# Kernel tuning notes

Measured on AMD Instinct MI355X. Metric: run time of the kernel, lower is better.

The kernel has to match this reference:

```python
import jax, jax.numpy as jnp
import numpy as np

B, T, D = 2, 2048, 2048
H, DK = 16, 96
DV = 192                 # head_v_dim = head_dim * expand_v (expand_v=2)
KEY_DIM = H * DK         # 1536 = 0.75*D
VAL_DIM = H * DV         # 3072 = 1.5*D
KS = 4                   # short-conv kernel size
EPS = 1e-6


def setup_inputs() -> dict:
    key = jax.random.key(0)
    ks = jax.random.split(key, 16)
    nrm = lambda k, shape, s: jax.random.normal(k, shape, jnp.float32) * s
    # dt_bias init as in the torch module
    dt_min, dt_max = 1e-3, 1e-1
    dt = jnp.exp(jax.random.uniform(ks[12], (H,), jnp.float32)
                 * (np.log(dt_max) - np.log(dt_min)) + np.log(dt_min))
    dt_bias = dt + jnp.log(-jnp.expm1(-dt))
    return {
        'x': nrm(ks[0], (B, T, D), 1.0),
        'Wq': nrm(ks[1], (D, KEY_DIM), D ** -0.5),
        'Wk': nrm(ks[2], (D, KEY_DIM), D ** -0.5),
        'Wv': nrm(ks[3], (D, VAL_DIM), D ** -0.5),
        'Wb': nrm(ks[4], (D, H), D ** -0.5),
        'Wa': nrm(ks[5], (D, H), D ** -0.5),
        'Wg': nrm(ks[6], (D, VAL_DIM), D ** -0.5),
        'Wo': nrm(ks[7], (VAL_DIM, D), VAL_DIM ** -0.5),
        'conv_q_w': nrm(ks[8], (KEY_DIM, KS), KS ** -0.5),
        'conv_k_w': nrm(ks[9], (KEY_DIM, KS), KS ** -0.5),
        'conv_v_w': nrm(ks[10], (VAL_DIM, KS), KS ** -0.5),
        'A_log': jnp.log(jax.random.uniform(ks[11], (H,), jnp.float32, 1e-4, 16.0)),
        'dt_bias': dt_bias,
        'o_norm_weight': jnp.ones((DV,), jnp.float32),
    }


def _causal_depthwise_conv(x, w):
    # x: (B, T, C), w: (C, KS). Depthwise causal conv + SiLU.
    xp = jnp.pad(x, ((0, 0), (KS - 1, 0), (0, 0)))
    y = sum(xp[:, j:j + T, :] * w[:, j] for j in range(KS))
    return jax.nn.silu(y)


def _gated_delta_scan(q, k, v, g, beta):
    # q,k: (B,T,H,DK)  v: (B,T,H,DV)  g,beta: (B,T,H)
    def step(S, inp):
        q_t, k_t, v_t, g_t, b_t = inp          # (B,H,DK),(B,H,DK),(B,H,DV),(B,H),(B,H)
        alpha = jnp.exp(g_t)                   # (B,H)
        retrieved = jnp.einsum('bhk,bhkv->bhv', k_t, S)
        error = v_t - retrieved                # (B,H,DV)
        S = alpha[:, :, None, None] * S + b_t[:, :, None, None] * (
            k_t[:, :, :, None] * error[:, :, None, :])
        o_t = jnp.einsum('bhk,bhkv->bhv', q_t, S)
        return S, o_t

    tm = lambda a: jnp.swapaxes(a, 0, 1)       # time-major
    S0 = jnp.zeros((B, H, DK, DV), jnp.float32)
    _, o = jax.lax.scan(step, S0, (tm(q), tm(k), tm(v), tm(g), tm(beta)))
    return jnp.swapaxes(o, 0, 1)               # (B,T,H,DV)


def reference(x, Wq, Wk, Wv, Wb, Wa, Wg, Wo,
              conv_q_w, conv_k_w, conv_v_w, A_log, dt_bias, o_norm_weight):
    # projections + causal depthwise short conv + SiLU
    q = _causal_depthwise_conv(x @ Wq, conv_q_w).reshape(B, T, H, DK)
    k = _causal_depthwise_conv(x @ Wk, conv_k_w).reshape(B, T, H, DK)
    v = _causal_depthwise_conv(x @ Wv, conv_v_w).reshape(B, T, H, DV)

    beta = jax.nn.sigmoid(x @ Wb)                                   # (B,T,H)
    g = -jnp.exp(A_log) * jax.nn.softplus(x @ Wa + dt_bias)         # (B,T,H)

    # qk L2 normalization (use_qk_l2norm_in_kernel=True path)
    q = q * jax.lax.rsqrt(jnp.sum(q * q, -1, keepdims=True) + 1e-12)
    k = k * jax.lax.rsqrt(jnp.sum(k * k, -1, keepdims=True) + 1e-12)

    o = _gated_delta_scan(q, k, v, g, beta)                         # (B,T,H,DV)

    # gated RMSNorm over head_v_dim
    g_out = (x @ Wg).reshape(B, T, H, DV)
    rms = jax.lax.rsqrt(jnp.mean(o * o, -1, keepdims=True) + EPS)
    o = (o * rms) * o_norm_weight * jax.nn.sigmoid(g_out)

    return o.reshape(B, T, VAL_DIM) @ Wo                            # (B,T,D)
```

## Files before the change

kernel.cpp:

```cpp
#include <hip/hip_runtime.h>

#define B_ 2
#define T_ 2048
#define D_ 2048
#define H_ 16
#define DK_ 96
#define DV_ 192
#define KEYD 1536
#define VALD 3072
#define NPROJ 9216
#define PQK 6144
#define KS_ 4
#define C_ 64
#define NC_ 32

typedef unsigned short u16;
typedef unsigned int u32;
typedef __bf16 bf16x8 __attribute__((ext_vector_type(8)));
typedef float f32x4 __attribute__((ext_vector_type(4)));

__device__ __forceinline__ u16 f2bf(float f) {
  unsigned u = __float_as_uint(f);
  u += 0x7FFF + ((u >> 16) & 1);
  return (u16)(u >> 16);
}
__device__ __forceinline__ float bf2f(u16 v) { return __uint_as_float((unsigned)v << 16); }
__device__ __forceinline__ float bflo(u32 w) { return __uint_as_float(w << 16); }
__device__ __forceinline__ float bfhi(u32 w) { return __uint_as_float(w & 0xFFFF0000u); }

__device__ __forceinline__ void gll16(const void* g, void* lds) {
  __builtin_amdgcn_global_load_lds(
      (const __attribute__((address_space(1))) void*)g,
      (__attribute__((address_space(3))) void*)lds, 16, 0, 0);
}

__global__ __launch_bounds__(256) void cast_x(const float* __restrict__ in,
                                              u16* __restrict__ out, int n4) {
  int i = blockIdx.x * 256 + threadIdx.x;
  if (i < n4) {
    float4 v = reinterpret_cast<const float4*>(in)[i];
    ushort4 o;
    o.x = f2bf(v.x); o.y = f2bf(v.y); o.z = f2bf(v.z); o.w = f2bf(v.w);
    reinterpret_cast<ushort4*>(out)[i] = o;
  }
}

__device__ __forceinline__ void tc_body(const float* __restrict__ src,
                                        u16* __restrict__ dst, int R, int C,
                                        int bx, int by, int tid) {
  __shared__ float tile[32][33];
  int tx = tid & 31, ty = tid >> 5;
  int c0 = bx * 32, r0 = by * 32;
#pragma unroll
  for (int j = 0; j < 4; ++j)
    tile[ty + j * 8][tx] = src[(size_t)(r0 + ty + j * 8) * C + c0 + tx];
  __syncthreads();
#pragma unroll
  for (int j = 0; j < 4; ++j)
    dst[(size_t)(c0 + ty + j * 8) * R + r0 + tx] = f2bf(tile[tx][ty + j * 8]);
}

__global__ __launch_bounds__(256) void transpose_cast(const float* __restrict__ src,
                                                      u16* __restrict__ dst, int R, int C) {
  tc_body(src, dst, R, C, blockIdx.x, blockIdx.y, threadIdx.x);
}

__global__ __launch_bounds__(256) void transpose_cast4(const float* __restrict__ Wq,
    const float* __restrict__ Wk, const float* __restrict__ Wv,
    const float* __restrict__ Wg, u16* __restrict__ WT) {
  int id = blockIdx.x;
  if (id < 3072) {
    tc_body(Wq, WT, 2048, 1536, id % 48, id / 48, threadIdx.x);
  } else if (id < 6144) {
    id -= 3072;
    tc_body(Wk, WT + (size_t)1536 * 2048, 2048, 1536, id % 48, id / 48, threadIdx.x);
  } else if (id < 12288) {
    id -= 6144;
    tc_body(Wv, WT + (size_t)3072 * 2048, 2048, 3072, id % 96, id / 96, threadIdx.x);
  } else {
    id -= 12288;
    tc_body(Wg, WT + (size_t)6144 * 2048, 2048, 3072, id % 96, id / 96, threadIdx.x);
  }
}

template <int OUT16>
__global__ __launch_bounds__(512, 2) void gemm256(const u16* __restrict__ A,
    const u16* __restrict__ BT, u16* __restrict__ C0, u16* __restrict__ C1,
    float* __restrict__ Cf, int M, int N, int K, int nsplit, int s0, int s1) {
  __shared__ u16 LA[2][256 * 64];
  __shared__ u16 LB[2][256 * 64];
  const int tid = threadIdx.x, wave = tid >> 6, lane = tid & 63;
  const int l15 = lane & 15, l16 = lane >> 4, x7 = l15 & 7;
  const int wr = wave >> 2, wc = wave & 3;
  const int m0 = blockIdx.y * 256, n0 = blockIdx.x * 256;
  const int r8 = lane >> 3;
  const int csrc = ((lane & 7) ^ r8) << 3;
  const int NKT = K >> 6;
  f32x4 acc[8][4] = {};

#define STG_A(p, kt, half) { \
    const u16* As_ = A + (size_t)m0 * K + (size_t)(kt) * 64; \
    _Pragma("unroll") \
    for (int g = 0; g < 2; ++g) { \
      int rowb = g * 128 + (half) * 64 + wave * 8; \
      gll16(As_ + (size_t)(rowb + r8) * K + csrc, (char*)&LA[p][0] + rowb * 128); \
    } \
  }
#define STG_B(p, kt) { \
    const u16* Bs_ = BT + (size_t)n0 * K + (size_t)(kt) * 64; \
    _Pragma("unroll") \
    for (int j = 0; j < 4; ++j) { \
      int rowb = j * 64 + wave * 8; \
      gll16(Bs_ + (size_t)(rowb + r8) * K + csrc, (char*)&LB[p][0] + rowb * 128); \
    } \
  }

#define LDA8(p, mh, dst) { \
    _Pragma("unroll") \
    for (int mi = 0; mi < 4; ++mi) \
      _Pragma("unroll") \
      for (int kk = 0; kk < 2; ++kk) { \
        int row = wr * 128 + (mh) * 64 + mi * 16 + l15; \
        dst[mi * 2 + kk] = *(const bf16x8*)((const char*)&LA[p][0] + row * 128 + (((kk * 4 + l16) ^ x7) << 4)); \
      } \
  }
#define LDB4(p, nh, dst) { \
    _Pragma("unroll") \
    for (int ni = 0; ni < 2; ++ni) \
      _Pragma("unroll") \
      for (int kk = 0; kk < 2; ++kk) { \
        int row = wc * 64 + (nh) * 32 + ni * 16 + l15; \
        dst[ni * 2 + kk] = *(const bf16x8*)((const char*)&LB[p][0] + row * 128 + (((kk * 4 + l16) ^ x7) << 4)); \
      } \
  }

#define MMQ(AF, BF, mbase, nbase) { \
    __builtin_amdgcn_s_setprio(1); \
    _Pragma("unroll") \
    for (int mi = 0; mi < 4; ++mi) \
      _Pragma("unroll") \
      for (int ni = 0; ni < 2; ++ni) \
        _Pragma("unroll") \
        for (int kk = 0; kk < 2; ++kk) \
          acc[(mbase) + mi][(nbase) + ni] = __builtin_amdgcn_mfma_f32_16x16x32_bf16( \
              AF[mi * 2 + kk], BF[ni * 2 + kk], acc[(mbase) + mi][(nbase) + ni], 0, 0, 0); \
    __builtin_amdgcn_s_setprio(0); \
  }

#define BARR() __builtin_amdgcn_s_barrier()

  STG_A(0, 0, 0); STG_A(0, 0, 1); STG_B(0, 0);
  if (NKT > 1) {
    STG_A(1, 1, 0); STG_A(1, 1, 1); STG_B(1, 1);
    asm volatile("s_waitcnt vmcnt(8)" ::: "memory");
  } else {
    asm volatile("s_waitcnt vmcnt(0)" ::: "memory");
  }
  BARR();

  bf16x8 afA[8], afB[8], bf0[4], bf1[4];
  for (int c = 0; c < NKT; ++c) {
    const int p = c & 1;
    const bool stg = (c + 2 < NKT);
    LDA8(p, 0, afA); LDB4(p, 0, bf0);
    BARR();
    MMQ(afA, bf0, 0, 0);
    BARR();
    LDB4(p, 1, bf1);
    if (stg) STG_A(p, c + 2, 0);
    BARR();
    MMQ(afA, bf1, 0, 2);
    BARR();
    LDA8(p, 1, afB);
    if (stg) STG_B(p, c + 2);
    BARR();
    MMQ(afB, bf1, 4, 2);
    BARR();
    if (stg) {
      STG_A(p, c + 2, 1);
      asm volatile("s_waitcnt vmcnt(8)" ::: "memory");
    } else if (c + 1 < NKT) {
      asm volatile("s_waitcnt vmcnt(0)" ::: "memory");
    }
    BARR();
    MMQ(afB, bf0, 4, 0);
    BARR();
  }

#pragma unroll
  for (int mi = 0; mi < 8; ++mi)
#pragma unroll
    for (int ni = 0; ni < 4; ++ni)
#pragma unroll
      for (int j = 0; j < 4; ++j) {
        int row = m0 + wr * 128 + mi * 16 + l16 * 4 + j;
        int col = n0 + wc * 64 + ni * 16 + l15;
        float v = acc[mi][ni][j];
        if (OUT16) {
          if (col < nsplit) C0[(size_t)row * s0 + col] = f2bf(v);
          else              C1[(size_t)row * s1 + col - nsplit] = f2bf(v);
        } else {
          Cf[(size_t)row * N + col] = v;
        }
      }
#undef STG_A
#undef STG_B
#undef LDA8
#undef LDB4
#undef MMQ
#undef BARR
}

template <int OUT16>
__global__ __launch_bounds__(256) void gemm_bt(const u16* __restrict__ A,
                                               const u16* __restrict__ BT,
                                               u16* __restrict__ C0, u16* __restrict__ C1,
                                               float* __restrict__ Cf,
                                               int M, int N, int K, int nsplit, int s0, int s1) {
  __shared__ u16 As[128 * 32];
  __shared__ u16 Bs[128 * 32];
  int tid = threadIdx.x;
  int wave = tid >> 6, lane = tid & 63;
  int l15 = lane & 15, l16 = lane >> 4;
  int m0 = blockIdx.y * 128, n0 = blockIdx.x * 128;
  int wm = (wave >> 1) * 64, wn = (wave & 1) * 64;
  f32x4 acc[4][4] = {};
  int nkt = K >> 5;
  for (int kt = 0; kt < nkt; ++kt) {
    int k0 = kt << 5;
    __syncthreads();
#pragma unroll
    for (int rr = 0; rr < 2; ++rr) {
      int idx = tid + rr * 256;
      int row = idx >> 2, kc8 = (idx & 3) * 8;
      unsigned loff = (unsigned)(rr * 256 + wave * 64) * 16;
      gll16(A + (size_t)(m0 + row) * K + k0 + kc8, (char*)As + loff);
      gll16(BT + (size_t)(n0 + row) * K + k0 + kc8, (char*)Bs + loff);
    }
    __syncthreads();
    bf16x8 af[4], bfr[4];
#pragma unroll
    for (int i = 0; i < 4; ++i)
      af[i] = *reinterpret_cast<const bf16x8*>(&As[(wm + i * 16 + l15) * 32 + l16 * 8]);
#pragma unroll
    for (int i = 0; i < 4; ++i)
      bfr[i] = *reinterpret_cast<const bf16x8*>(&Bs[(wn + i * 16 + l15) * 32 + l16 * 8]);
#pragma unroll
    for (int mi = 0; mi < 4; ++mi)
#pragma unroll
      for (int ni = 0; ni < 4; ++ni)
        acc[mi][ni] = __builtin_amdgcn_mfma_f32_16x16x32_bf16(af[mi], bfr[ni], acc[mi][ni], 0, 0, 0);
  }
#pragma unroll
  for (int mi = 0; mi < 4; ++mi)
#pragma unroll
    for (int ni = 0; ni < 4; ++ni)
#pragma unroll
      for (int j = 0; j < 4; ++j) {
        int row = m0 + wm + mi * 16 + l16 * 4 + j;
        int col = n0 + wn + ni * 16 + l15;
        if (OUT16) {
          if (col < nsplit) C0[(size_t)row * s0 + col] = f2bf(acc[mi][ni][j]);
          else              C1[(size_t)row * s1 + col - nsplit] = f2bf(acc[mi][ni][j]);
        } else {
          Cf[(size_t)row * N + col] = acc[mi][ni][j];
        }
      }
}

__global__ __launch_bounds__(256) void proj_bg(const float* __restrict__ x,
    const float* __restrict__ Wb, const float* __restrict__ Wa,
    const float* __restrict__ A_log, const float* __restrict__ dt_bias,
    float* __restrict__ beta, float* __restrict__ gg) {
  __shared__ float xs[4 * 2048];
  __shared__ float red[4][32][8];
  int tid = threadIdx.x;
  int r0 = blockIdx.x * 4;
  for (int i = tid; i < 4 * 2048; i += 256)
    xs[i] = x[(size_t)r0 * D_ + i];
  __syncthreads();
  int colg = tid & 31, ks = tid >> 5;
  const float* W = (colg < 16) ? Wb : Wa;
  int wc = colg & 15;
  float p0 = 0, p1 = 0, p2 = 0, p3 = 0;
  int kbeg = ks * 256;
  for (int k = kbeg; k < kbeg + 256; ++k) {
    float wv = W[k * H_ + wc];
    p0 += xs[k] * wv;
    p1 += xs[2048 + k] * wv;
    p2 += xs[4096 + k] * wv;
    p3 += xs[6144 + k] * wv;
  }
  red[0][colg][ks] = p0; red[1][colg][ks] = p1;
  red[2][colg][ks] = p2; red[3][colg][ks] = p3;
  __syncthreads();
  if (tid < 128) {
    int row = tid >> 5, col = tid & 31;
    float d = 0;
#pragma unroll
    for (int i = 0; i < 8; ++i) d += red[row][col][i];
    int r = r0 + row;
    if (col < 16) {
      beta[(size_t)r * H_ + col] = 1.f / (1.f + __expf(-d));
    } else {
      int hh = col - 16;
      float z = d + dt_bias[hh];
      float sp = (z > 20.f) ? z : log1pf(__expf(z));
      gg[(size_t)r * H_ + hh] = -__expf(A_log[hh]) * sp;
    }
  }
}

__global__ __launch_bounds__(256) void conv_qkv(const u16* __restrict__ Pqkv,
    const float* __restrict__ wq, const float* __restrict__ wk, const float* __restrict__ wv,
    u16* __restrict__ qc, u16* __restrict__ kc, u16* __restrict__ vc) {
  __shared__ __align__(16) u16 rows[4][PQK];
  int bt = blockIdx.x;
  int t = bt & (T_ - 1);
  int tid = threadIdx.x, h = tid >> 4, li = tid & 15;
#pragma unroll
  for (int r = 0; r < 4; ++r) {
    bool valid = (t + r - 3) >= 0;
    const uint4* src = (const uint4*)(Pqkv + (ptrdiff_t)(bt + r - 3) * PQK);
    uint4* dst = (uint4*)rows[r];
#pragma unroll
    for (int i = 0; i < 3; ++i) {
      int off = tid + i * 256;
      uint4 v;
      if (valid) v = src[off];
      else { v.x = 0; v.y = 0; v.z = 0; v.w = 0; }
      dst[off] = v;
    }
  }
  __syncthreads();

#pragma unroll
  for (int part = 0; part < 2; ++part) {
    const float* w = part ? wk : wq;
    float y[6]; float ss = 0.f;
#pragma unroll
    for (int jj = 0; jj < 6; ++jj) {
      int c = li + jj * 16;
      int ch = h * DK_ + c;
      float a = 0.f;
#pragma unroll
      for (int j = 0; j < KS_; ++j)
        a += bf2f(rows[j][part * KEYD + ch]) * w[ch * KS_ + j];
      float yv = a / (1.f + __expf(-a));
      y[jj] = yv; ss += yv * yv;
    }
    ss += __shfl_xor(ss, 1); ss += __shfl_xor(ss, 2);
    ss += __shfl_xor(ss, 4); ss += __shfl_xor(ss, 8);
    float rn = rsqrtf(ss + 1e-12f);
    u16* out = (part ? kc : qc) + (size_t)bt * KEYD + h * DK_;
#pragma unroll
    for (int jj = 0; jj < 6; ++jj) out[li + jj * 16] = f2bf(y[jj] * rn);
  }
  u16* vout = vc + (size_t)bt * VALD;
#pragma unroll
  for (int jj = 0; jj < 12; ++jj) {
    int c = tid + jj * 256;
    float a = 0.f;
#pragma unroll
    for (int j = 0; j < KS_; ++j)
      a += bf2f(rows[j][2 * KEYD + c]) * wv[c * KS_ + j];
    vout[c] = f2bf(a / (1.f + __expf(-a)));
  }
}

__global__ __launch_bounds__(320) void chunk_prep(
    const u16* __restrict__ kc, u16* __restrict__ Uv ,
    const float* __restrict__ gg, const float* __restrict__ beta,
    u16* __restrict__ Wg, float* __restrict__ Gcum,
    float* __restrict__ cdArr, float* __restrict__ lamArr) {
  __shared__ __align__(16) u16 ktL[64 * 104];
  __shared__ float AmL[64 * 68];
  __shared__ float glL[64], GclL[64], blL[64], DplL[64];
  int tid = threadIdx.x;
  int flat = blockIdx.x;
  int c = flat & 31, bh = flat >> 5, h = bh & 15, b = bh >> 4;
  int bT0 = b * T_ + c * 64;

  {
    const u32* kg = (const u32*)(kc + (size_t)bT0 * KEYD + h * DK_);
    for (int i = tid; i < 3072; i += 320) {
      int t = i / 48, dd = i - t * 48;
      ((u32*)ktL)[t * 52 + dd] = kg[(size_t)t * (KEYD / 2) + dd];
    }
  }
  if (tid < 64) {
    float g = gg[(size_t)(bT0 + tid) * H_ + h];
    float bv = beta[(size_t)(bT0 + tid) * H_ + h];
    float v = g;
#pragma unroll
    for (int off = 1; off < 64; off <<= 1) {
      float u = __shfl_up(v, off);
      if (tid >= off) v += u;
    }
    float g63 = __shfl(v, 63);
    glL[tid] = g; GclL[tid] = v; blL[tid] = bv; DplL[tid] = __expf(v - g);
    Gcum[(size_t)flat * 64 + tid] = v;
    cdArr[(size_t)flat * 64 + tid] = bv * __expf(g63 - v);
    if (tid == 63) lamArr[flat] = __expf(v);
  }
  __syncthreads();

  {
    int wave = tid >> 6, lane = tid & 63, l15 = lane & 15, l16 = lane >> 4;
    if (wave < 4) {
      f32x4 ac[4] = {};
#pragma unroll
      for (int ks = 0; ks < 3; ++ks) {
        bf16x8 a = *(const bf16x8*)&ktL[(wave * 16 + l15) * 104 + ks * 32 + l16 * 8];
#pragma unroll
        for (int n = 0; n < 4; ++n) {
          bf16x8 bb = *(const bf16x8*)&ktL[(n * 16 + l15) * 104 + ks * 32 + l16 * 8];
          ac[n] = __builtin_amdgcn_mfma_f32_16x16x32_bf16(a, bb, ac[n], 0, 0, 0);
        }
      }
#pragma unroll
      for (int n = 0; n < 4; ++n)
#pragma unroll
        for (int j = 0; j < 4; ++j) {
          int t = wave * 16 + l16 * 4 + j;
          int jj = n * 16 + l15;
          float val = 0.f;
          if (jj < t) val = __expf((GclL[t] - glL[t]) - GclL[jj]) * blL[jj] * ac[n][j];
          AmL[t * 68 + jj] = val;
        }
    }
  }
  __syncthreads();

  if (tid < 288) {
    int j = tid;
    float m[64];
    if (j < 192) {
      const u16* up = Uv + (size_t)bT0 * VALD + h * DV_ + j;
#pragma unroll
      for (int t = 0; t < 64; ++t) m[t] = bf2f(up[(size_t)t * VALD]);
    } else {
      int d = j - 192;
#pragma unroll
      for (int t = 0; t < 64; ++t) m[t] = DplL[t] * bf2f(ktL[t * 104 + d]);
    }
#pragma unroll
    for (int t0 = 0; t0 < 64; t0 += 4) {
      {
        f32x4 a1 = *(const f32x4*)&AmL[(t0 + 1) * 68 + t0];
        m[t0 + 1] -= a1[0] * m[t0];
        f32x4 a2 = *(const f32x4*)&AmL[(t0 + 2) * 68 + t0];
        m[t0 + 2] -= a2[0] * m[t0] + a2[1] * m[t0 + 1];
        f32x4 a3 = *(const f32x4*)&AmL[(t0 + 3) * 68 + t0];
        m[t0 + 3] -= a3[0] * m[t0] + a3[1] * m[t0 + 1] + a3[2] * m[t0 + 2];
      }
#pragma unroll
      for (int tp = t0 + 4; tp < 64; ++tp) {
        f32x4 a = *(const f32x4*)&AmL[tp * 68 + t0];
        m[tp] -= a[0] * m[t0] + a[1] * m[t0 + 1] + a[2] * m[t0 + 2] + a[3] * m[t0 + 3];
      }
    }
    if (j < 192) {
      u16* up = Uv + (size_t)bT0 * VALD + h * DV_ + j;
#pragma unroll
      for (int t = 0; t < 64; ++t) up[(size_t)t * VALD] = f2bf(m[t]);
    } else {
      int d = j - 192;
      u16* wp = Wg + (size_t)bT0 * KEYD + h * DK_ + d;
#pragma unroll
      for (int t = 0; t < 64; ++t) wp[(size_t)t * KEYD] = f2bf(m[t]);
    }
  }
}

__global__ __launch_bounds__(256) void serial_state(
    const u16* __restrict__ kc, const u16* __restrict__ Wg, u16* __restrict__ Ue,
    const float* __restrict__ cdArr, const float* __restrict__ lamArr,
    u16* __restrict__ Schk) {
  __shared__ __align__(16) u16 WtL[2][64 * 104];
  __shared__ __align__(16) u16 ktT[2][96 * 72];
  __shared__ __align__(16) u16 StH[32 * 104];
  __shared__ __align__(16) u16 StLo[32 * 104];
  __shared__ __align__(16) u16 EtH[32 * 72];
  __shared__ __align__(16) u16 EtLo[32 * 72];
  __shared__ float lamS[2];

  int tid = threadIdx.x, wave = tid >> 6, lane = tid & 63;
  int l15 = lane & 15, l16 = lane >> 4;
  int jq = blockIdx.x % 6, bh = blockIdx.x / 6, h = bh & 15, b = bh >> 4;
  int col0 = jq * 32;
  int ntS = wave & 1, m3 = 3 * (wave >> 1);
  int st_t = tid >> 2, st_dd = (tid & 3) * 12;

  f32x4 Sf[3] = {};
  uint4 wreg[3], kreg[3];
  u16 ureg[2][4];
  float cdv[4];
  float lamReg;

#define PREFETCH(bT0p, flatp) { \
    const u32* wgp = (const u32*)(Wg + (size_t)((bT0p) + st_t) * KEYD + h * DK_) + st_dd; \
    const u32* kgp = (const u32*)(kc + (size_t)((bT0p) + st_t) * KEYD + h * DK_) + st_dd; \
    wreg[0] = ((const uint4*)wgp)[0]; wreg[1] = ((const uint4*)wgp)[1]; wreg[2] = ((const uint4*)wgp)[2]; \
    kreg[0] = ((const uint4*)kgp)[0]; kreg[1] = ((const uint4*)kgp)[1]; kreg[2] = ((const uint4*)kgp)[2]; \
    _Pragma("unroll") \
    for (int ni = 0; ni < 2; ++ni) \
      _Pragma("unroll") \
      for (int j = 0; j < 4; ++j) \
        ureg[ni][j] = Ue[(size_t)((bT0p) + wave * 16 + l16 * 4 + j) * VALD + h * DV_ + col0 + ni * 16 + l15]; \
    _Pragma("unroll") \
    for (int j = 0; j < 4; ++j) cdv[j] = cdArr[(size_t)(flatp) * 64 + wave * 16 + l16 * 4 + j]; \
    if (tid == 0) lamReg = lamArr[flatp]; \
  }

  PREFETCH(b * T_, bh * NC_);

  for (int c = 0; c < NC_; ++c) {
    int buf = c & 1;
    int flat = bh * NC_ + c;
    int bT0 = b * T_ + (c << 6);
    {
      u32* wl = (u32*)&WtL[buf][0] + st_t * 52 + st_dd;
      ((uint4*)wl)[0] = wreg[0];
      *(uint4*)(wl + 4) = wreg[1];
      *(uint4*)(wl + 8) = wreg[2];
#pragma unroll
      for (int r = 0; r < 3; ++r) {
        u32 vals[4] = {kreg[r].x, kreg[r].y, kreg[r].z, kreg[r].w};
#pragma unroll
        for (int e = 0; e < 4; ++e) {
          int d = 2 * (st_dd + r * 4 + e);
          ktT[buf][d * 72 + st_t] = (u16)(vals[e] & 0xFFFFu);
          ktT[buf][(d + 1) * 72 + st_t] = (u16)(vals[e] >> 16);
        }
      }
      int cl = ntS * 16 + l15;
      u16* schkRow = Schk + (size_t)flat * (DK_ * DV_) + (size_t)(col0 + cl) * DK_;
#pragma unroll
      for (int i = 0; i < 3; ++i) {
        u16 hi0 = f2bf(Sf[i][0]), hi1 = f2bf(Sf[i][1]);
        u16 hi2 = f2bf(Sf[i][2]), hi3 = f2bf(Sf[i][3]);
        int dbase = (m3 + i) * 16 + l16 * 4;
        StH[cl * 104 + dbase + 0] = hi0; StLo[cl * 104 + dbase + 0] = f2bf(Sf[i][0] - bf2f(hi0));
        StH[cl * 104 + dbase + 1] = hi1; StLo[cl * 104 + dbase + 1] = f2bf(Sf[i][1] - bf2f(hi1));
        StH[cl * 104 + dbase + 2] = hi2; StLo[cl * 104 + dbase + 2] = f2bf(Sf[i][2] - bf2f(hi2));
        StH[cl * 104 + dbase + 3] = hi3; StLo[cl * 104 + dbase + 3] = f2bf(Sf[i][3] - bf2f(hi3));
        u32* ow = (u32*)(schkRow + dbase);
        ow[0] = ((u32)hi1 << 16) | hi0;
        ow[1] = ((u32)hi3 << 16) | hi2;
      }
      if (tid == 0) lamS[buf] = lamReg;
    }
    __syncthreads();
    {
      f32x4 Ea[2] = {};
#pragma unroll
      for (int ks = 0; ks < 3; ++ks) {
        bf16x8 a = *(const bf16x8*)&WtL[buf][(wave * 16 + l15) * 104 + ks * 32 + l16 * 8];
#pragma unroll
        for (int ni = 0; ni < 2; ++ni) {
          bf16x8 bhv = *(const bf16x8*)&StH[(ni * 16 + l15) * 104 + ks * 32 + l16 * 8];
          bf16x8 blv = *(const bf16x8*)&StLo[(ni * 16 + l15) * 104 + ks * 32 + l16 * 8];
          Ea[ni] = __builtin_amdgcn_mfma_f32_16x16x32_bf16(a, bhv, Ea[ni], 0, 0, 0);
          Ea[ni] = __builtin_amdgcn_mfma_f32_16x16x32_bf16(a, blv, Ea[ni], 0, 0, 0);
        }
      }
#pragma unroll
      for (int ni = 0; ni < 2; ++ni)
#pragma unroll
        for (int j = 0; j < 4; ++j) {
          int t = wave * 16 + l16 * 4 + j;
          float ev = bf2f(ureg[ni][j]) - Ea[ni][j];
          Ue[(size_t)(bT0 + t) * VALD + h * DV_ + col0 + ni * 16 + l15] = f2bf(ev);
          float ep = cdv[j] * ev;
          u16 ehi = f2bf(ep);
          int cl = ni * 16 + l15;
          EtH[cl * 72 + t] = ehi;
          EtLo[cl * 72 + t] = f2bf(ep - bf2f(ehi));
        }
      if (c + 1 < NC_) PREFETCH(bT0 + 64, flat + 1);
    }
    __syncthreads();
    {
      float lam = lamS[buf];
#pragma unroll
      for (int i = 0; i < 3; ++i)
#pragma unroll
        for (int j = 0; j < 4; ++j) Sf[i][j] *= lam;
#pragma unroll
      for (int ks = 0; ks < 2; ++ks) {
        bf16x8 bhv = *(const bf16x8*)&EtH[(ntS * 16 + l15) * 72 + ks * 32 + l16 * 8];
        bf16x8 blv = *(const bf16x8*)&EtLo[(ntS * 16 + l15) * 72 + ks * 32 + l16 * 8];
#pragma unroll
        for (int i = 0; i < 3; ++i) {
          bf16x8 a = *(const bf16x8*)&ktT[buf][((m3 + i) * 16 + l15) * 72 + ks * 32 + l16 * 8];
          Sf[i] = __builtin_amdgcn_mfma_f32_16x16x32_bf16(a, bhv, Sf[i], 0, 0, 0);
          Sf[i] = __builtin_amdgcn_mfma_f32_16x16x32_bf16(a, blv, Sf[i], 0, 0, 0);
        }
      }
    }
  }
#undef PREFETCH
}

__global__ __launch_bounds__(256) void chunk_out(
    const u16* __restrict__ qc, const u16* __restrict__ kc, const u16* __restrict__ Ee,
    const u16* __restrict__ Schk, const float* __restrict__ Gcum,
    const float* __restrict__ beta, const u16* __restrict__ Pg,
    const float* __restrict__ onw, u16* __restrict__ onb) {
  __shared__ __align__(16) char pool[65280];
  u16* qL   = (u16*)pool;
  u16* BmL  = (u16*)(pool + 12288);
  u16* BmLo = (u16*)(pool + 21504);
  u16* kL   = (u16*)(pool + 30720);
  u16* StL  = (u16*)(pool + 30720);
  u16* EtL  = (u16*)(pool + 50688);
  float* GclL = (float*)(pool + 64512);
  float* blL  = (float*)(pool + 64768);
  float* DlL  = (float*)(pool + 65024);
  u16* PgL  = (u16*)pool;
  float* wL = (float*)(pool + 24576);

  int tid = threadIdx.x, wave = tid >> 6, lane = tid & 63;
  int l15 = lane & 15, l16 = lane >> 4;
  int flat = blockIdx.x;
  int c = flat & 31, bh = flat >> 5, h = bh & 15, b = bh >> 4;
  int bT0 = b * T_ + c * 64;

  {
    const u32* qg = (const u32*)(qc + (size_t)bT0 * KEYD + h * DK_);
    const u32* kg = (const u32*)(kc + (size_t)bT0 * KEYD + h * DK_);
    for (int i = tid; i < 3072; i += 256) {
      int t = i / 48, dd = i - t * 48;
      ((u32*)qL)[t * 48 + dd] = qg[(size_t)t * (KEYD / 2) + dd];
      ((u32*)kL)[t * 48 + dd] = kg[(size_t)t * (KEYD / 2) + dd];
    }
    if (tid < 64) {
      float gv = Gcum[(size_t)flat * 64 + tid];
      GclL[tid] = gv;
      DlL[tid] = __expf(gv);
      blL[tid] = beta[(size_t)(bT0 + tid) * H_ + h];
    }
  }
  __syncthreads();

  {
    f32x4 bacc[4] = {};
#pragma unroll
    for (int kk = 0; kk < 3; ++kk) {
      bf16x8 aq = *(const bf16x8*)&qL[(wave * 16 + l15) * 96 + kk * 32 + l16 * 8];
#pragma unroll
      for (int n = 0; n < 4; ++n) {
        bf16x8 bk = *(const bf16x8*)&kL[(n * 16 + l15) * 96 + kk * 32 + l16 * 8];
        bacc[n] = __builtin_amdgcn_mfma_f32_16x16x32_bf16(aq, bk, bacc[n], 0, 0, 0);
      }
    }
#pragma unroll
    for (int n = 0; n < 4; ++n)
#pragma unroll
      for (int j = 0; j < 4; ++j) {
        int t = wave * 16 + l16 * 4 + j;
        int jj = n * 16 + l15;
        float val = 0.f;
        if (jj <= t) val = __expf(GclL[t] - GclL[jj]) * blL[jj] * bacc[n][j];
        u16 hi = f2bf(val);
        BmL[t * 72 + jj] = hi;
        BmLo[t * 72 + jj] = f2bf(val - bf2f(hi));
      }
  }
  __syncthreads();

  f32x4 oacc0[6] = {};
  f32x4 oacc1[6] = {};

#define HALFC(half, OACC) { \
    { \
      const u32* sg = (const u32*)(Schk + (size_t)flat * (DK_ * DV_) + (size_t)((half) * 96) * DK_); \
      for (int i = tid; i < 4608; i += 256) { \
        int cL = i / 48, dd = i - cL * 48; \
        ((u32*)&StL[cL * 104])[dd] = sg[cL * 48 + dd]; \
      } \
      const u32* eg = (const u32*)(Ee + (size_t)bT0 * VALD + h * DV_ + (half) * 96); \
      for (int i = tid; i < 3072; i += 256) { \
        int t = i / 48, dd = i - t * 48; \
        u32 w2 = eg[(size_t)t * (VALD / 2) + dd]; \
        EtL[(2 * dd) * 72 + t]     = (u16)(w2 & 0xFFFF); \
        EtL[(2 * dd + 1) * 72 + t] = (u16)(w2 >> 16); \
      } \
    } \
    __syncthreads(); \
    _Pragma("unroll") \
    for (int kk = 0; kk < 3; ++kk) { \
      bf16x8 aq = *(const bf16x8*)&qL[(wave * 16 + l15) * 96 + kk * 32 + l16 * 8]; \
      _Pragma("unroll") \
      for (int n = 0; n < 6; ++n) { \
        bf16x8 bs = *(const bf16x8*)&StL[(n * 16 + l15) * 104 + kk * 32 + l16 * 8]; \
        OACC[n] = __builtin_amdgcn_mfma_f32_16x16x32_bf16(aq, bs, OACC[n], 0, 0, 0); \
      } \
    } \
    _Pragma("unroll") \
    for (int n = 0; n < 6; ++n) \
      _Pragma("unroll") \
      for (int j = 0; j < 4; ++j) \
        OACC[n][j] *= DlL[wave * 16 + l16 * 4 + j]; \
    _Pragma("unroll") \
    for (int kk = 0; kk < 2; ++kk) { \
      bf16x8 ah = *(const bf16x8*)&BmL[(wave * 16 + l15) * 72 + kk * 32 + l16 * 8]; \
      bf16x8 al = *(const bf16x8*)&BmLo[(wave * 16 + l15) * 72 + kk * 32 + l16 * 8]; \
      _Pragma("unroll") \
      for (int n = 0; n < 6; ++n) { \
        bf16x8 be = *(const bf16x8*)&EtL[(n * 16 + l15) * 72 + kk * 32 + l16 * 8]; \
        OACC[n] = __builtin_amdgcn_mfma_f32_16x16x32_bf16(ah, be, OACC[n], 0, 0, 0); \
        OACC[n] = __builtin_amdgcn_mfma_f32_16x16x32_bf16(al, be, OACC[n], 0, 0, 0); \
      } \
    } \
    __syncthreads(); \
  }

  HALFC(0, oacc0);
  HALFC(1, oacc1);
#undef HALFC

  {
    const uint4* pgg = (const uint4*)(Pg + (size_t)bT0 * VALD + h * DV_);
    int tr = tid >> 2, q = tid & 3;
    uint4* dstRow = (uint4*)&PgL[tr * 192];
    const uint4* srcRow = (const uint4*)((const u16*)pgg + (size_t)tr * VALD);
#pragma unroll
    for (int ii = 0; ii < 6; ++ii)
      dstRow[q * 6 + ii] = srcRow[q * 6 + ii];
    if (tid < 192) wL[tid] = onw[tid];
  }
  __syncthreads();

  float ssv[4] = {0.f, 0.f, 0.f, 0.f};
#pragma unroll
  for (int n = 0; n < 6; ++n)
#pragma unroll
    for (int j = 0; j < 4; ++j) {
      float y0 = bf2f(f2bf(oacc0[n][j]));
      float y1 = bf2f(f2bf(oacc1[n][j]));
      ssv[j] += y0 * y0 + y1 * y1;
    }
#pragma unroll
  for (int j = 0; j < 4; ++j) {
    ssv[j] += __shfl_xor(ssv[j], 1); ssv[j] += __shfl_xor(ssv[j], 2);
    ssv[j] += __shfl_xor(ssv[j], 4); ssv[j] += __shfl_xor(ssv[j], 8);
  }
  float rmsv[4];
#pragma unroll
  for (int j = 0; j < 4; ++j) rmsv[j] = rsqrtf(ssv[j] * (1.f / DV_) + 1e-6f);

#define EPIL(OACC, half) { \
    _Pragma("unroll") \
    for (int n = 0; n < 6; ++n) \
      _Pragma("unroll") \
      for (int j = 0; j < 4; ++j) { \
        int t = wave * 16 + l16 * 4 + j; \
        int cc = (half) * 96 + n * 16 + l15; \
        float yv = bf2f(f2bf(OACC[n][j])); \
        float gv = bf2f(PgL[t * 192 + cc]); \
        float sig = 1.f / (1.f + __expf(-gv)); \
        onb[(size_t)(bT0 + t) * VALD + h * DV_ + cc] = f2bf(yv * rmsv[j] * wL[cc] * sig); \
      } \
  }
  EPIL(oacc0, 0);
  EPIL(oacc1, 1);
#undef EPIL
}

extern "C" void kernel_launch(void* const* d_in, const int* in_sizes, int n_in,
                              void* d_out, int out_size, void* d_ws, size_t ws_size,
                              hipStream_t stream) {
  (void)in_sizes; (void)n_in; (void)out_size; (void)ws_size;
  const float* x      = (const float*)d_in[0];
  const float* Wq     = (const float*)d_in[1];
  const float* Wk     = (const float*)d_in[2];
  const float* Wv     = (const float*)d_in[3];
  const float* Wb     = (const float*)d_in[4];
  const float* Wa     = (const float*)d_in[5];
  const float* Wg     = (const float*)d_in[6];
  const float* Wo     = (const float*)d_in[7];
  const float* cqw    = (const float*)d_in[8];
  const float* ckw    = (const float*)d_in[9];
  const float* cvw    = (const float*)d_in[10];
  const float* A_log  = (const float*)d_in[11];
  const float* dt_bias= (const float*)d_in[12];
  const float* onw    = (const float*)d_in[13];
  float* out = (float*)d_out;

  char* ws = (char*)d_ws;
  u16*   xb    = (u16*)  (ws + 0);
  u16*   WT    = (u16*)  (ws + 16777216);
  u16*   qc    = (u16*)  (ws + 0);
  u16*   kc    = (u16*)  (ws + 12582912);
  u16*   vc    = (u16*)  (ws + 25165824);
  u16*   Pqkv  = (u16*)  (ws + 54525952);
  u16*   Wbuf  = (u16*)  (ws + 54525952);
  u16*   Schk  = (u16*)  (ws + 67108864);
  u16*   Pg    = (u16*)  (ws + 104857600);
  float* beta  = (float*)(ws + 155189248);
  float* gg    = (float*)(ws + 155451392);
  float* Gcum  = (float*)(ws + 155713536);
  float* cdArr = (float*)(ws + 155975680);
  float* lamArr= (float*)(ws + 156237824);
  u16*   onb   = (u16*)  (ws + 54525952);
  u16*   WoT   = (u16*)  (ws + 79691776);

  int n4 = B_ * T_ * D_ / 4;
  cast_x<<<(n4 + 255) / 256, 256, 0, stream>>>(x, xb, n4);
  transpose_cast4<<<18432, 256, 0, stream>>>(Wq, Wk, Wv, Wg, WT);

  gemm256<1><<<dim3(NPROJ / 256, (B_ * T_) / 256), 512, 0, stream>>>(
      xb, WT, Pqkv, Pg, nullptr, B_ * T_, NPROJ, D_, PQK, PQK, VALD);
  proj_bg<<<(B_ * T_) / 4, 256, 0, stream>>>(x, Wb, Wa, A_log, dt_bias, beta, gg);
  conv_qkv<<<B_ * T_, 256, 0, stream>>>(Pqkv, cqw, ckw, cvw, qc, kc, vc);

  chunk_prep<<<B_ * H_ * NC_, 320, 0, stream>>>(kc, vc, gg, beta, Wbuf, Gcum, cdArr, lamArr);
  serial_state<<<B_ * H_ * 6, 256, 0, stream>>>(kc, Wbuf, vc, cdArr, lamArr, Schk);
  chunk_out<<<B_ * H_ * NC_, 256, 0, stream>>>(qc, kc, vc, Schk, Gcum, beta, Pg, onw, onb);

  transpose_cast<<<dim3(64, 96), 256, 0, stream>>>(Wo, WoT, 3072, 2048);
  gemm_bt<0><<<dim3(D_ / 128, (B_ * T_) / 128), 256, 0, stream>>>(
      onb, WoT, nullptr, nullptr, out, B_ * T_, D_, VALD, 0, 0, 0);
}
```

Baseline: 566.2 us.

## Split serial state scan across twice as many blocks and fuse x cast into weight transpose

The serial chunk-state kernel now gives each block 16 value columns instead of 32, so the grid grows from 192 to 384 blocks and each block's sequential chain over chunks does less MFMA work per step. The 96 key rows are split as six 16-row tiles over four waves, so two waves handle an extra tile and the work is uneven across waves. The K/W tiles are still loaded per block, so those global loads double overall. Separately, the x-to-bf16 cast is folded into the weight transpose launch to drop one kernel launch.

```diff
diff --git a/kernel.cpp b/kernel.cpp
--- a/kernel.cpp
+++ b/kernel.cpp
@@ -34,17 +34,6 @@
       (__attribute__((address_space(3))) void*)lds, 16, 0, 0);
 }
 
-__global__ __launch_bounds__(256) void cast_x(const float* __restrict__ in,
-                                              u16* __restrict__ out, int n4) {
-  int i = blockIdx.x * 256 + threadIdx.x;
-  if (i < n4) {
-    float4 v = reinterpret_cast<const float4*>(in)[i];
-    ushort4 o;
-    o.x = f2bf(v.x); o.y = f2bf(v.y); o.z = f2bf(v.z); o.w = f2bf(v.w);
-    reinterpret_cast<ushort4*>(out)[i] = o;
-  }
-}
-
 __device__ __forceinline__ void tc_body(const float* __restrict__ src,
                                         u16* __restrict__ dst, int R, int C,
                                         int bx, int by, int tid) {
@@ -67,7 +56,8 @@
 
 __global__ __launch_bounds__(256) void transpose_cast4(const float* __restrict__ Wq,
     const float* __restrict__ Wk, const float* __restrict__ Wv,
-    const float* __restrict__ Wg, u16* __restrict__ WT) {
+    const float* __restrict__ Wg, u16* __restrict__ WT,
+    const float* __restrict__ x, u16* __restrict__ xb, int n4) {
   int id = blockIdx.x;
   if (id < 3072) {
     tc_body(Wq, WT, 2048, 1536, id % 48, id / 48, threadIdx.x);
@@ -77,9 +67,17 @@
   } else if (id < 12288) {
     id -= 6144;
     tc_body(Wv, WT + (size_t)3072 * 2048, 2048, 3072, id % 96, id / 96, threadIdx.x);
-  } else {
+  } else if (id < 18432) {
     id -= 12288;
     tc_body(Wg, WT + (size_t)6144 * 2048, 2048, 3072, id % 96, id / 96, threadIdx.x);
+  } else {
+    int i = (id - 18432) * 256 + threadIdx.x;
+    if (i < n4) {
+      float4 v = reinterpret_cast<const float4*>(x)[i];
+      ushort4 o;
+      o.x = f2bf(v.x); o.y = f2bf(v.y); o.z = f2bf(v.z); o.w = f2bf(v.w);
+      reinterpret_cast<ushort4*>(xb)[i] = o;
+    }
   }
 }
 
@@ -479,22 +477,24 @@
     u16* __restrict__ Schk) {
   __shared__ __align__(16) u16 WtL[2][64 * 104];
   __shared__ __align__(16) u16 ktT[2][96 * 72];
-  __shared__ __align__(16) u16 StH[32 * 104];
-  __shared__ __align__(16) u16 StLo[32 * 104];
-  __shared__ __align__(16) u16 EtH[32 * 72];
-  __shared__ __align__(16) u16 EtLo[32 * 72];
+  __shared__ __align__(16) u16 StH[16 * 104];
+  __shared__ __align__(16) u16 StLo[16 * 104];
+  __shared__ __align__(16) u16 EtH[16 * 72];
+  __shared__ __align__(16) u16 EtLo[16 * 72];
   __shared__ float lamS[2];
 
   int tid = threadIdx.x, wave = tid >> 6, lane = tid & 63;
   int l15 = lane & 15, l16 = lane >> 4;
-  int jq = blockIdx.x % 6, bh = blockIdx.x / 6, h = bh & 15, b = bh >> 4;
-  int col0 = jq * 32;
-  int ntS = wave & 1, m3 = 3 * (wave >> 1);
+  int sl = blockIdx.x % 12, bh = blockIdx.x / 12, h = bh & 15, b = bh >> 4;
+  int col0 = sl * 16;
   int st_t = tid >> 2, st_dd = (tid & 3) * 12;
-
-  f32x4 Sf[3] = {};
+  const bool hasB = (wave < 2);
+  const int dtA = wave, dtB = 4 + wave;
+
+  f32x4 Sf0 = {};
+  f32x4 Sf1 = {};
   uint4 wreg[3], kreg[3];
-  u16 ureg[2][4];
+  u16 ureg[4];
   float cdv[4];
   float lamReg;
 
@@ -504,10 +504,8 @@
     wreg[0] = ((const uint4*)wgp)[0]; wreg[1] = ((const uint4*)wgp)[1]; wreg[2] = ((const uint4*)wgp)[2]; \
     kreg[0] = ((const uint4*)kgp)[0]; kreg[1] = ((const uint4*)kgp)[1]; kreg[2] = ((const uint4*)kgp)[2]; \
     _Pragma("unroll") \
-    for (int ni = 0; ni < 2; ++ni) \
-      _Pragma("unroll") \
-      for (int j = 0; j < 4; ++j) \
-        ureg[ni][j] = Ue[(size_t)((bT0p) + wave * 16 + l16 * 4 + j) * VALD + h * DV_ + col0 + ni * 16 + l15]; \
+    for (int j = 0; j < 4; ++j) \
+      ureg[j] = Ue[(size_t)((bT0p) + wave * 16 + l16 * 4 + j) * VALD + h * DV_ + col0 + l15]; \
     _Pragma("unroll") \
     for (int j = 0; j < 4; ++j) cdv[j] = cdArr[(size_t)(flatp) * 64 + wave * 16 + l16 * 4 + j]; \
     if (tid == 0) lamReg = lamArr[flatp]; \
@@ -534,68 +532,76 @@
           ktT[buf][(d + 1) * 72 + st_t] = (u16)(vals[e] >> 16);
         }
       }
-      int cl = ntS * 16 + l15;
-      u16* schkRow = Schk + (size_t)flat * (DK_ * DV_) + (size_t)(col0 + cl) * DK_;
-#pragma unroll
-      for (int i = 0; i < 3; ++i) {
-        u16 hi0 = f2bf(Sf[i][0]), hi1 = f2bf(Sf[i][1]);
-        u16 hi2 = f2bf(Sf[i][2]), hi3 = f2bf(Sf[i][3]);
-        int dbase = (m3 + i) * 16 + l16 * 4;
-        StH[cl * 104 + dbase + 0] = hi0; StLo[cl * 104 + dbase + 0] = f2bf(Sf[i][0] - bf2f(hi0));
-        StH[cl * 104 + dbase + 1] = hi1; StLo[cl * 104 + dbase + 1] = f2bf(Sf[i][1] - bf2f(hi1));
-        StH[cl * 104 + dbase + 2] = hi2; StLo[cl * 104 + dbase + 2] = f2bf(Sf[i][2] - bf2f(hi2));
-        StH[cl * 104 + dbase + 3] = hi3; StLo[cl * 104 + dbase + 3] = f2bf(Sf[i][3] - bf2f(hi3));
+      u16* schkRow = Schk + (size_t)flat * (DK_ * DV_) + (size_t)(col0 + l15) * DK_;
+      {
+        u16 hi0 = f2bf(Sf0[0]), hi1 = f2bf(Sf0[1]);
+        u16 hi2 = f2bf(Sf0[2]), hi3 = f2bf(Sf0[3]);
+        int dbase = dtA * 16 + l16 * 4;
+        StH[l15 * 104 + dbase + 0] = hi0; StLo[l15 * 104 + dbase + 0] = f2bf(Sf0[0] - bf2f(hi0));
+        StH[l15 * 104 + dbase + 1] = hi1; StLo[l15 * 104 + dbase + 1] = f2bf(Sf0[1] - bf2f(hi1));
+        StH[l15 * 104 + dbase + 2] = hi2; StLo[l15 * 104 + dbase + 2] = f2bf(Sf0[2] - bf2f(hi2));
+        StH[l15 * 104 + dbase + 3] = hi3; StLo[l15 * 104 + dbase + 3] = f2bf(Sf0[3] - bf2f(hi3));
         u32* ow = (u32*)(schkRow + dbase);
         ow[0] = ((u32)hi1 << 16) | hi0;
         ow[1] = ((u32)hi3 << 16) | hi2;
       }
+      if (hasB) {
+        u16 hi0 = f2bf(Sf1[0]), hi1 = f2bf(Sf1[1]);
+        u16 hi2 = f2bf(Sf1[2]), hi3 = f2bf(Sf1[3]);
+        int dbase = dtB * 16 + l16 * 4;
+        StH[l15 * 104 + dbase + 0] = hi0; StLo[l15 * 104 + dbase + 0] = f2bf(Sf1[0] - bf2f(hi0));
+        StH[l15 * 104 + dbase + 1] = hi1; StLo[l15 * 104 + dbase + 1] = f2bf(Sf1[1] - bf2f(hi1));
+        StH[l15 * 104 + dbase + 2] = hi2; StLo[l15 * 104 + dbase + 2] = f2bf(Sf1[2] - bf2f(hi2));
+        StH[l15 * 104 + dbase + 3] = hi3; StLo[l15 * 104 + dbase + 3] = f2bf(Sf1[3] - bf2f(hi3));
+        u32* ow = (u32*)(schkRow + dbase);
+        ow[0] = ((u32)hi1 << 16) | hi0;
+        ow[1] = ((u32)hi3 << 16) | hi2;
+      }
       if (tid == 0) lamS[buf] = lamReg;
     }
     __syncthreads();
     {
-      f32x4 Ea[2] = {};
+      f32x4 Ea = {};
 #pragma unroll
       for (int ks = 0; ks < 3; ++ks) {
         bf16x8 a = *(const bf16x8*)&WtL[buf][(wave * 16 + l15) * 104 + ks * 32 + l16 * 8];
-#pragma unroll
-        for (int ni = 0; ni < 2; ++ni) {
-          bf16x8 bhv = *(const bf16x8*)&StH[(ni * 16 + l15) * 104 + ks * 32 + l16 * 8];
-          bf16x8 blv = *(const bf16x8*)&StLo[(ni * 16 + l15) * 104 + ks * 32 + l16 * 8];
-          Ea[ni] = __builtin_amdgcn_mfma_f32_16x16x32_bf16(a, bhv, Ea[ni], 0, 0, 0);
-          Ea[ni] = __builtin_amdgcn_mfma_f32_16x16x32_bf16(a, blv, Ea[ni], 0, 0, 0);
-        }
-      }
-#pragma unroll
-      for (int ni = 0; ni < 2; ++ni)
-#pragma unroll
-        for (int j = 0; j < 4; ++j) {
-          int t = wave * 16 + l16 * 4 + j;
-          float ev = bf2f(ureg[ni][j]) - Ea[ni][j];
-          Ue[(size_t)(bT0 + t) * VALD + h * DV_ + col0 + ni * 16 + l15] = f2bf(ev);
-          float ep = cdv[j] * ev;
-          u16 ehi = f2bf(ep);
-          int cl = ni * 16 + l15;
-          EtH[cl * 72 + t] = ehi;
-          EtLo[cl * 72 + t] = f2bf(ep - bf2f(ehi));
-        }
+        bf16x8 bhv = *(const bf16x8*)&StH[l15 * 104 + ks * 32 + l16 * 8];
+        bf16x8 blv = *(const bf16x8*)&StLo[l15 * 104 + ks * 32 + l16 * 8];
+        Ea = __builtin_amdgcn_mfma_f32_16x16x32_bf16(a, bhv, Ea, 0, 0, 0);
+        Ea = __builtin_amdgcn_mfma_f32_16x16x32_bf16(a, blv, Ea, 0, 0, 0);
+      }
+#pragma unroll
+      for (int j = 0; j < 4; ++j) {
+        int t = wave * 16 + l16 * 4 + j;
+        float ev = bf2f(ureg[j]) - Ea[j];
+        Ue[(size_t)(bT0 + t) * VALD + h * DV_ + col0 + l15] = f2bf(ev);
+        float ep = cdv[j] * ev;
+        u16 ehi = f2bf(ep);
+        EtH[l15 * 72 + t] = ehi;
+        EtLo[l15 * 72 + t] = f2bf(ep - bf2f(ehi));
+      }
       if (c + 1 < NC_) PREFETCH(bT0 + 64, flat + 1);
     }
     __syncthreads();
     {
       float lam = lamS[buf];
 #pragma unroll
-      for (int i = 0; i < 3; ++i)
-#pragma unroll
-        for (int j = 0; j < 4; ++j) Sf[i][j] *= lam;
+      for (int j = 0; j < 4; ++j) Sf0[j] *= lam;
+      if (hasB) {
+#pragma unroll
+        for (int j = 0; j < 4; ++j) Sf1[j] *= lam;
+      }
 #pragma unroll
       for (int ks = 0; ks < 2; ++ks) {
-        bf16x8 bhv = *(const bf16x8*)&EtH[(ntS * 16 + l15) * 72 + ks * 32 + l16 * 8];
-        bf16x8 blv = *(const bf16x8*)&EtLo[(ntS * 16 + l15) * 72 + ks * 32 + l16 * 8];
-#pragma unroll
-        for (int i = 0; i < 3; ++i) {
-          bf16x8 a = *(const bf16x8*)&ktT[buf][((m3 + i) * 16 + l15) * 72 + ks * 32 + l16 * 8];
-          Sf[i] = __builtin_amdgcn_mfma_f32_16x16x32_bf16(a, bhv, Sf[i], 0, 0, 0);
-          Sf[i] = __builtin_amdgcn_mfma_f32_16x16x32_bf16(a, blv, Sf[i], 0, 0, 0);
+        bf16x8 bhv = *(const bf16x8*)&EtH[l15 * 72 + ks * 32 + l16 * 8];
+        bf16x8 blv = *(const bf16x8*)&EtLo[l15 * 72 + ks * 32 + l16 * 8];
+        bf16x8 aA = *(const bf16x8*)&ktT[buf][(dtA * 16 + l15) * 72 + ks * 32 + l16 * 8];
+        Sf0 = __builtin_amdgcn_mfma_f32_16x16x32_bf16(aA, bhv, Sf0, 0, 0, 0);
+        Sf0 = __builtin_amdgcn_mfma_f32_16x16x32_bf16(aA, blv, Sf0, 0, 0, 0);
+        if (hasB) {
+          bf16x8 aB = *(const bf16x8*)&ktT[buf][(dtB * 16 + l15) * 72 + ks * 32 + l16 * 8];
+          Sf1 = __builtin_amdgcn_mfma_f32_16x16x32_bf16(aB, bhv, Sf1, 0, 0, 0);
+          Sf1 = __builtin_amdgcn_mfma_f32_16x16x32_bf16(aB, blv, Sf1, 0, 0, 0);
         }
       }
     }
@@ -808,8 +814,7 @@
   u16*   WoT   = (u16*)  (ws + 79691776);
 
   int n4 = B_ * T_ * D_ / 4;
-  cast_x<<<(n4 + 255) / 256, 256, 0, stream>>>(x, xb, n4);
-  transpose_cast4<<<18432, 256, 0, stream>>>(Wq, Wk, Wv, Wg, WT);
+  transpose_cast4<<<18432 + (n4 + 255) / 256, 256, 0, stream>>>(Wq, Wk, Wv, Wg, WT, x, xb, n4);
 
   gemm256<1><<<dim3(NPROJ / 256, (B_ * T_) / 256), 512, 0, stream>>>(
       xb, WT, Pqkv, Pg, nullptr, B_ * T_, NPROJ, D_, PQK, PQK, VALD);
@@ -817,7 +822,7 @@
   conv_qkv<<<B_ * T_, 256, 0, stream>>>(Pqkv, cqw, ckw, cvw, qc, kc, vc);
 
   chunk_prep<<<B_ * H_ * NC_, 320, 0, stream>>>(kc, vc, gg, beta, Wbuf, Gcum, cdArr, lamArr);
-  serial_state<<<B_ * H_ * 6, 256, 0, stream>>>(kc, Wbuf, vc, cdArr, lamArr, Schk);
+  serial_state<<<B_ * H_ * 12, 256, 0, stream>>>(kc, Wbuf, vc, cdArr, lamArr, Schk);
   chunk_out<<<B_ * H_ * NC_, 256, 0, stream>>>(qc, kc, vc, Schk, Gcum, beta, Pg, onw, onb);
 
   transpose_cast<<<dim3(64, 96), 256, 0, stream>>>(Wo, WoT, 3072, 2048);
```

Measured after the change: 584.8 us. 3.3% more time.
